# Kernel tuning notes

Hardware: AMD Instinct MI355X
Metric: run time of the kernel (lower is better)

Reference implementation:

```python
import math
import jax, jax.numpy as jnp
import numpy as np

DIM, HEADS, HD = 384, 12, 32
FEAT, WIN, SHIFT = (64, 64), (8, 8), (4, 4)
L = WIN[0] * WIN[1]  # window area = 64
MAX_LOGIT = math.log(1.0 / 0.01)


def _rel_log_coords():
    # pair-wise relative positions, log-spaced (static, numpy)
    coords = np.stack(np.meshgrid(np.arange(WIN[0]), np.arange(WIN[1]), indexing='ij'), 0).reshape(2, -1)
    rel = (coords[:, :, None] - coords[:, None, :]).transpose(1, 2, 0).reshape(-1, 2).astype(np.float32)
    return np.sign(rel) * np.log1p(np.abs(rel))  # [L*L, 2]


def _attn_mask():
    # shifted-window attention mask (static, numpy): 9 regions -> -100 across regions
    H, W = FEAT
    img = np.zeros((H, W), np.int32)
    cnt = 0
    for h0, h1 in ((0, H - WIN[0]), (H - WIN[0], H - SHIFT[0]), (H - SHIFT[0], H)):
        for w0, w1 in ((0, W - WIN[1]), (W - WIN[1], W - SHIFT[1]), (W - SHIFT[1], W)):
            img[h0:h1, w0:w1] = cnt
            cnt += 1
    mw = img.reshape(H // WIN[0], WIN[0], W // WIN[1], WIN[1]).transpose(0, 2, 1, 3).reshape(-1, L)
    diff = mw[:, None, :] - mw[:, :, None]
    return np.where(diff != 0, -100.0, 0.0).astype(np.float32)  # [nW, L, L]


def _ln(x, w, b, eps=1e-5):
    mu = x.mean(-1, keepdims=True)
    var = ((x - mu) ** 2).mean(-1, keepdims=True)
    return (x - mu) / jnp.sqrt(var + eps) * w + b


def setup_inputs() -> dict:
    key = jax.random.key(0)
    ks = jax.random.split(key, 12)
    B = 32
    s = 0.02
    return {
        'x': jax.random.normal(ks[0], (B, FEAT[0], FEAT[1], DIM), jnp.float32),
        'qkv_w': jax.random.normal(ks[1], (3 * DIM, DIM), jnp.float32) * s,
        'qkv_b': jnp.zeros((3 * DIM,), jnp.float32),
        'proj_w': jax.random.normal(ks[2], (DIM, DIM), jnp.float32) * s,
        'proj_b': jnp.zeros((DIM,), jnp.float32),
        'meta_w1': jax.random.normal(ks[3], (384, 2), jnp.float32) * 0.1,
        'meta_b1': jnp.zeros((384,), jnp.float32),
        'meta_w2': jax.random.normal(ks[4], (HEADS, 384), jnp.float32) * 0.1,
        'meta_b2': jnp.zeros((HEADS,), jnp.float32),
        'logit_scale': jnp.full((HEADS,), math.log(10.0), jnp.float32),
        'norm1_w': jnp.ones((DIM,), jnp.float32),
        'norm1_b': jnp.zeros((DIM,), jnp.float32),
        'fc1_w': jax.random.normal(ks[5], (4 * DIM, DIM), jnp.float32) * s,
        'fc1_b': jnp.zeros((4 * DIM,), jnp.float32),
        'fc2_w': jax.random.normal(ks[6], (DIM, 4 * DIM), jnp.float32) * s,
        'fc2_b': jnp.zeros((DIM,), jnp.float32),
        'norm2_w': jnp.ones((DIM,), jnp.float32),
        'norm2_b': jnp.zeros((DIM,), jnp.float32),
    }


def reference(x, qkv_w, qkv_b, proj_w, proj_b, meta_w1, meta_b1, meta_w2, meta_b2,
              logit_scale, norm1_w, norm1_b, fc1_w, fc1_b, fc2_w, fc2_b, norm2_w, norm2_b):
    B, H, W, C = x.shape
    wh, ww = WIN
    # cyclic shift + window partition: (B,H,W,C) -> (B*nW, L, C)
    sx = jnp.roll(x, (-SHIFT[0], -SHIFT[1]), axis=(1, 2))
    xw = sx.reshape(B, H // wh, wh, W // ww, ww, C).transpose(0, 1, 3, 2, 4, 5).reshape(-1, L, C)
    Bw = xw.shape[0]
    qkv = (xw @ qkv_w.T + qkv_b).reshape(Bw, L, 3, HEADS, HD).transpose(2, 0, 3, 1, 4)
    q, k, v = qkv[0], qkv[1], qkv[2]  # [Bw, heads, L, hd]
    # cosine attention
    qn = q / jnp.maximum(jnp.linalg.norm(q, axis=-1, keepdims=True), 1e-12)
    kn = k / jnp.maximum(jnp.linalg.norm(k, axis=-1, keepdims=True), 1e-12)
    attn = jnp.einsum('bhqd,bhkd->bhqk', qn, kn)
    scale = jnp.exp(jnp.minimum(logit_scale, MAX_LOGIT)).reshape(1, HEADS, 1, 1)
    # MLP-based relative position bias
    rel = jnp.asarray(_rel_log_coords())
    bias = jax.nn.relu(rel @ meta_w1.T + meta_b1) @ meta_w2.T + meta_b2  # [L*L, heads]
    bias = bias.T.reshape(HEADS, L, L)
    attn = attn * scale + bias[None]
    # shift mask
    mask = jnp.asarray(_attn_mask())  # [nW, L, L]
    nW = mask.shape[0]
    attn = attn.reshape(Bw // nW, nW, HEADS, L, L) + mask[None, :, None]
    attn = jax.nn.softmax(attn.reshape(Bw, HEADS, L, L), axis=-1)
    out = jnp.einsum('bhqk,bhkd->bhqd', attn, v).transpose(0, 2, 1, 3).reshape(Bw, L, C)
    out = out @ proj_w.T + proj_b
    # window reverse + reverse shift
    out = out.reshape(B, H // wh, W // ww, wh, ww, C).transpose(0, 1, 3, 2, 4, 5).reshape(B, H, W, C)
    out = jnp.roll(out, (SHIFT[0], SHIFT[1]), axis=(1, 2))
    # post-norm residuals (SwinV2Cr style)
    x = x + _ln(out, norm1_w, norm1_b)
    h = jax.nn.gelu(x @ fc1_w.T + fc1_b, approximate=False) @ fc2_w.T + fc2_b
    x = x + _ln(h, norm2_w, norm2_b)
    return x
```

## Files before the change

kernel.cpp:

```cpp
#include <hip/hip_runtime.h>
#include <hip/hip_bf16.h>

typedef __attribute__((ext_vector_type(4))) float f32x4;
typedef __attribute__((ext_vector_type(4))) unsigned int u32x4;
typedef __attribute__((ext_vector_type(8))) __bf16 bf16x8;

#define DEV static __device__ __forceinline__

DEV unsigned short f2bf(float f) {
  unsigned u = __builtin_bit_cast(unsigned, f);
  u += 0x7fffu + ((u >> 16) & 1u);
  return (unsigned short)(u >> 16);
}
DEV float bf2f(unsigned short b) {
  return __builtin_bit_cast(float, ((unsigned)b) << 16);
}
DEV unsigned pk2(float a, float b) {
  return (unsigned)f2bf(a) | ((unsigned)f2bf(b) << 16);
}
DEV unsigned cvtpk(float lo, float hi) {
  unsigned r;
  asm("v_cvt_pk_bf16_f32 %0, %1, %2" : "=v"(r) : "v"(lo), "v"(hi));
  return r;
}
DEV float fexp2(float x) {
  float r;
  asm("v_exp_f32 %0, %1" : "=v"(r) : "v"(x));
  return r;
}
DEV f32x4 mfma16(u32x4 a, u32x4 b, f32x4 c) {
  return __builtin_amdgcn_mfma_f32_16x16x32_bf16(
      __builtin_bit_cast(bf16x8, a), __builtin_bit_cast(bf16x8, b), c, 0, 0, 0);
}
DEV float ssq8(u32x4 c) {
  float s = 0.f;
#pragma unroll
  for (int e = 0; e < 4; e++) {
    float lo = __builtin_bit_cast(float, c[e] << 16);
    float hi = __builtin_bit_cast(float, c[e] & 0xffff0000u);
    s += lo * lo + hi * hi;
  }
  return s;
}
DEV void gload16(const unsigned short* g, unsigned short* l) {
  __builtin_amdgcn_global_load_lds(
      (const __attribute__((address_space(1))) unsigned int*)g,
      (__attribute__((address_space(3))) unsigned int*)l, 16, 0, 0);
}

template <int EPI>
__global__ __launch_bounds__(512, 2) void gemm8(
    const unsigned short* __restrict__ A, const unsigned short* __restrict__ B,
    const float* __restrict__ bias, unsigned short* __restrict__ C,
    int Nc, int K, int nblocks) {
  __shared__ __align__(16) unsigned char smem[131072];
  unsigned short* As0 = (unsigned short*)smem;
  unsigned short* Bs0 = (unsigned short*)(smem + 65536);
  const int bid = blockIdx.x;
  const int mchunk = (gridDim.x >> 3) / nblocks;
  const int xcd = bid & 7, idx = bid >> 3;
  const int nb = idx % nblocks, ml = idx / nblocks;
  const int m0 = (xcd * mchunk + ml) * 256, n0 = nb * 256;
  const int tid = threadIdx.x, w = tid >> 6, l = tid & 63;
  const int lr = l & 15, lg = l >> 4;
  const int wm = (w >> 2) * 128, wn = (w & 3) * 64;
  const int srow = l >> 3;
  const int scol = ((l & 7) ^ srow) * 8;
  const int NT = K >> 6;

  auto stA = [&](int p, int kt, int half, int j) {
    int r = half * 128 + w * 16 + j * 8;
    gload16(A + (size_t)(m0 + r + srow) * K + kt * 64 + scol,
            As0 + p * 16384 + r * 64);
  };
  auto stB = [&](int p, int kt, int half, int j) {
    int r = half * 128 + w * 16 + j * 8;
    gload16(B + (size_t)(n0 + r + srow) * K + kt * 64 + scol,
            Bs0 + p * 16384 + r * 64);
  };

  const f32x4 z4 = {0.f, 0.f, 0.f, 0.f};
  f32x4 acc[8][4];
#pragma unroll
  for (int i = 0; i < 8; i++)
#pragma unroll
    for (int j = 0; j < 4; j++) acc[i][j] = z4;
  u32x4 af[8], bf[8];

#pragma unroll
  for (int ktp = 0; ktp < 2; ktp++) {
    stB(ktp, ktp, 0, 0); stB(ktp, ktp, 0, 1);
    stB(ktp, ktp, 1, 0); stB(ktp, ktp, 1, 1);
    stA(ktp, ktp, 0, 0); stA(ktp, ktp, 0, 1);
    stA(ktp, ktp, 1, 0); stA(ktp, ktp, 1, 1);
  }

  for (int kt = 0; kt < NT; ++kt) {
    const int p = kt & 1;
    if (kt + 1 < NT) {
      asm volatile("s_waitcnt vmcnt(8)" ::: "memory");
    } else {
      asm volatile("s_waitcnt vmcnt(0)" ::: "memory");
    }
    __builtin_amdgcn_s_barrier();

#pragma unroll
    for (int ni = 0; ni < 4; ni++)
#pragma unroll
      for (int ks = 0; ks < 2; ks++) {
        int R = wn + ni * 16 + lr;
        bf[ni * 2 + ks] = *(const u32x4*)&Bs0[p * 16384 + R * 64 +
                                             (((ks * 4 + lg) ^ (lr & 7)) * 8)];
      }
#pragma unroll
    for (int mi = 0; mi < 4; mi++)
#pragma unroll
      for (int ks = 0; ks < 2; ks++) {
        int R = wm + mi * 16 + lr;
        af[mi * 2 + ks] = *(const u32x4*)&As0[p * 16384 + R * 64 +
                                              (((ks * 4 + lg) ^ (lr & 7)) * 8)];
      }
    asm volatile("s_waitcnt lgkmcnt(0)" ::: "memory");
    __builtin_amdgcn_sched_barrier(0);
    __builtin_amdgcn_s_setprio(1);
#pragma unroll
    for (int mi = 0; mi < 4; mi++)
#pragma unroll
      for (int ni = 0; ni < 2; ni++)
#pragma unroll
        for (int ks = 0; ks < 2; ks++)
          acc[mi][ni] = mfma16(bf[ni * 2 + ks], af[mi * 2 + ks], acc[mi][ni]);
    __builtin_amdgcn_s_setprio(0);
    __builtin_amdgcn_s_barrier();

    if (kt + 2 < NT) { stB(p, kt + 2, 0, 0); stB(p, kt + 2, 0, 1); }
    __builtin_amdgcn_s_setprio(1);
#pragma unroll
    for (int mi = 0; mi < 4; mi++)
#pragma unroll
      for (int ni = 0; ni < 2; ni++)
#pragma unroll
        for (int ks = 0; ks < 2; ks++)
          acc[mi][ni + 2] =
              mfma16(bf[(ni + 2) * 2 + ks], af[mi * 2 + ks], acc[mi][ni + 2]);
    __builtin_amdgcn_s_setprio(0);
    __builtin_amdgcn_s_barrier();

#pragma unroll
    for (int mi = 0; mi < 4; mi++)
#pragma unroll
      for (int ks = 0; ks < 2; ks++) {
        int R = wm + 64 + mi * 16 + lr;
        af[mi * 2 + ks] = *(const u32x4*)&As0[p * 16384 + R * 64 +
                                              (((ks * 4 + lg) ^ (lr & 7)) * 8)];
      }
    if (kt + 2 < NT) { stB(p, kt + 2, 1, 0); stB(p, kt + 2, 1, 1); }
    asm volatile("s_waitcnt lgkmcnt(0)" ::: "memory");
    __builtin_amdgcn_sched_barrier(0);
    __builtin_amdgcn_s_setprio(1);
#pragma unroll
    for (int mi = 0; mi < 4; mi++)
#pragma unroll
      for (int ni = 0; ni < 2; ni++)
#pragma unroll
        for (int ks = 0; ks < 2; ks++)
          acc[mi + 4][ni] =
              mfma16(bf[ni * 2 + ks], af[mi * 2 + ks], acc[mi + 4][ni]);
    __builtin_amdgcn_s_setprio(0);
    __builtin_amdgcn_s_barrier();

    if (kt + 2 < NT) {
      stA(p, kt + 2, 0, 0); stA(p, kt + 2, 0, 1);
      stA(p, kt + 2, 1, 0); stA(p, kt + 2, 1, 1);
    }
    __builtin_amdgcn_s_setprio(1);
#pragma unroll
    for (int mi = 0; mi < 4; mi++)
#pragma unroll
      for (int ni = 0; ni < 2; ni++)
#pragma unroll
        for (int ks = 0; ks < 2; ks++)
          acc[mi + 4][ni + 2] =
              mfma16(bf[(ni + 2) * 2 + ks], af[mi * 2 + ks], acc[mi + 4][ni + 2]);
    __builtin_amdgcn_s_setprio(0);
  }

  __builtin_amdgcn_s_barrier();
#pragma unroll
  for (int mh = 0; mh < 2; mh++)
#pragma unroll
    for (int mi = 0; mi < 4; mi++) {
      int mloc = wm + mh * 64 + mi * 16 + lr;
      int msw = mloc & 7;
#pragma unroll
      for (int ni = 0; ni < 4; ni++) {
        f32x4 v = acc[mh * 4 + mi][ni];
        f32x4 bv = *(const f32x4*)&bias[n0 + wn + ni * 16 + lg * 4];
#pragma unroll
        for (int r = 0; r < 4; r++) {
          float t = v[r] + bv[r];
          if (EPI == 1) t = 0.5f * t * (1.0f + erff(t * 0.70710678f));
          v[r] = t;
        }
        int nbyte = (wn + ni * 16 + lg * 4) * 2;
        int addr = mloc * 512 + ((((nbyte >> 4) ^ msw) << 4) | (nbyte & 8));
        *(uint2*)(smem + addr) = make_uint2(cvtpk(v[0], v[1]), cvtpk(v[2], v[3]));
      }
    }
  __syncthreads();
#pragma unroll
  for (int c = 0; c < 16; c++) {
    int m = w * 32 + c * 2 + (l >> 5);
    int h = l & 31;
    u32x4 v = *(const u32x4*)(smem + m * 512 + ((h ^ (m & 7)) << 4));
    int n = n0 + h * 8;
    if (n < Nc) *(u32x4*)&C[(size_t)(m0 + m) * Nc + n] = v;
  }
}

template <int MODE>
__global__ __launch_bounds__(512) void gemm_ln(
    const unsigned short* __restrict__ A, const unsigned short* __restrict__ Bw,
    const float* __restrict__ bias, const float* __restrict__ resf,
    const unsigned short* __restrict__ resb, const float* __restrict__ nw,
    const float* __restrict__ nb, unsigned short* __restrict__ outb,
    float* __restrict__ outf, int K) {
  __shared__ __align__(16) unsigned short As[2][4096];
  __shared__ __align__(16) unsigned short Bs[2][12288];
  const int bid = blockIdx.x;
  const int swz = (bid & 7) * (gridDim.x >> 3) + (bid >> 3);
  const int m0 = swz * 128;
  const int tid = threadIdx.x, w8 = tid >> 6, l = tid & 63;
  const int lr = l & 15, lg = l >> 4;
  const int gsw = (lg ^ ((lr >> 1) & 3)) * 8;
  const int wm2 = (w8 >> 2) * 64;
  const int wn4 = w8 & 3;

  const int rs = l >> 2;
  const int gsrc = ((l & 3) ^ ((l >> 3) & 3)) * 8;
  const unsigned short* g_src[4];
  unsigned short* g_dst[4];
  int g_str[4];
#pragma unroll
  for (int i = 0; i < 4; i++) {
    int g = w8 * 4 + i;
    if (g < 8) {
      g_src[i] = A + (size_t)(m0 + g * 16 + rs) * K + gsrc;
      g_dst[i] = &As[0][g * 512];
      g_str[i] = 4096;
    } else {
      g_src[i] = Bw + (size_t)((g - 8) * 16 + rs) * K + gsrc;
      g_dst[i] = &Bs[0][(g - 8) * 512];
      g_str[i] = 12288;
    }
  }
  auto stage = [&](int buf, int k0) {
#pragma unroll
    for (int i = 0; i < 4; i++) gload16(g_src[i] + k0, g_dst[i] + buf * g_str[i]);
  };

  const f32x4 z4 = {0.f, 0.f, 0.f, 0.f};
  f32x4 acc[4][6];
#pragma unroll
  for (int i = 0; i < 4; i++)
#pragma unroll
    for (int j = 0; j < 6; j++) acc[i][j] = z4;

  auto compute = [&](int buf) {
    u32x4 a[4], b[6];
#pragma unroll
    for (int i = 0; i < 4; i++)
      a[i] = *(const u32x4*)(&As[buf][(wm2 + i * 16 + lr) * 32 + gsw]);
#pragma unroll
    for (int j = 0; j < 6; j++)
      b[j] = *(const u32x4*)(&Bs[buf][(wn4 * 96 + j * 16 + lr) * 32 + gsw]);
#pragma unroll
    for (int i = 0; i < 4; i++)
#pragma unroll
      for (int j = 0; j < 6; j++) acc[i][j] = mfma16(a[i], b[j], acc[i][j]);
  };

  const int nt = K >> 5;
  stage(0, 0);
  for (int t = 0; t < nt; ++t) {
    __syncthreads();
    if (t + 1 < nt) stage((t + 1) & 1, (t + 1) * 32);
    compute(t & 1);
  }

  float bcol[6];
#pragma unroll
  for (int j = 0; j < 6; j++) bcol[j] = bias[wn4 * 96 + j * 16 + lr];
#pragma unroll
  for (int i = 0; i < 4; i++)
#pragma unroll
    for (int j = 0; j < 6; j++)
#pragma unroll
      for (int r = 0; r < 4; r++) acc[i][j][r] += bcol[j];

  float* psum = (float*)(&As[0][0]);
  float* psq  = (float*)(&As[0][1024]);
#pragma unroll
  for (int i = 0; i < 4; i++)
#pragma unroll
    for (int r = 0; r < 4; r++) {
      float s1 = 0.f, s2 = 0.f;
#pragma unroll
      for (int j = 0; j < 6; j++) {
        float v = acc[i][j][r];
        s1 += v;
        s2 += v * v;
      }
#pragma unroll
      for (int d = 1; d < 16; d <<= 1) {
        s1 += __shfl_xor(s1, d, 64);
        s2 += __shfl_xor(s2, d, 64);
      }
      if (lr == 0) {
        int row = wm2 + i * 16 + lg * 4 + r;
        psum[wn4 * 128 + row] = s1;
        psq[wn4 * 128 + row] = s2;
      }
    }
  __syncthreads();

  float wcol[6], b2col[6];
#pragma unroll
  for (int j = 0; j < 6; j++) {
    int col = wn4 * 96 + j * 16 + lr;
    wcol[j] = nw[col];
    b2col[j] = nb[col];
  }
#pragma unroll
  for (int i = 0; i < 4; i++)
#pragma unroll
    for (int r = 0; r < 4; r++) {
      int row = wm2 + i * 16 + lg * 4 + r;
      float sum = psum[row] + psum[128 + row] + psum[256 + row] + psum[384 + row];
      float sq = psq[row] + psq[128 + row] + psq[256 + row] + psq[384 + row];
      float mu = sum * (1.f / 384.f);
      float rstd = rsqrtf(sq * (1.f / 384.f) - mu * mu + 1e-5f);
      size_t nbase;
      if (MODE == 0) {
        int mrow = m0 + row;
        int bb = mrow >> 12, widx = (mrow >> 6) & 63, tt = mrow & 63;
        int yy = (((widx >> 3) << 3) + (tt >> 3) + 4) & 63;
        int xx = (((widx & 7) << 3) + (tt & 7) + 4) & 63;
        nbase = (size_t)((bb << 12) | (yy << 6) | xx) * 384;
      } else {
        nbase = (size_t)(m0 + row) * 384;
      }
#pragma unroll
      for (int j = 0; j < 6; j++) {
        int col = wn4 * 96 + j * 16 + lr;
        float v = (acc[i][j][r] - mu) * rstd * wcol[j] + b2col[j];
        if (MODE == 0) {
          outb[nbase + col] = f2bf(resf[nbase + col] + v);
        } else {
          outf[nbase + col] = bf2f(resb[nbase + col]) + v;
        }
      }
    }
}

__global__ __launch_bounds__(256) void gather_cvt(
    const float* __restrict__ x, unsigned short* __restrict__ xb) {
  int wv = threadIdx.x >> 6, l = threadIdx.x & 63;
  int m = blockIdx.x * 4 + wv;
  int w = m >> 6, t = m & 63;
  int b = w >> 6, wy = (w >> 3) & 7, wx = w & 7;
  int oy = (wy * 8 + (t >> 3) + 4) & 63;
  int ox = (wx * 8 + (t & 7) + 4) & 63;
  const float2* src =
      (const float2*)(x + (size_t)((((b << 6) | oy) << 6) | ox) * 384 + l * 6);
  float2 f0 = src[0], f1 = src[1], f2 = src[2];
  unsigned* dst = (unsigned*)(xb + (size_t)m * 384 + l * 6);
  dst[0] = pk2(f0.x, f0.y);
  dst[1] = pk2(f1.x, f1.y);
  dst[2] = pk2(f2.x, f2.y);
}

__global__ __launch_bounds__(256, 4) void attn_win(
    const unsigned short* __restrict__ qkv, const float* __restrict__ btab2,
    const float* __restrict__ lscale, unsigned short* __restrict__ aout) {
  __shared__ __align__(16) unsigned short vT[4][32 * 72];
  __shared__ __align__(16) float rnk[4][64];
  const int w = blockIdx.x;
  const int wv = threadIdx.x >> 6, l = threadIdx.x & 63;
  const int h = blockIdx.y * 4 + wv;
  const int lr = l & 15, lg = l >> 4;
  const size_t base = (size_t)w * 64 * 1152 + h * 32;
  const f32x4 z4 = {0.f, 0.f, 0.f, 0.f};

  {
    const u32x4* vp = (const u32x4*)(qkv + base + (size_t)l * 1152 + 768);
#pragma unroll
    for (int c4 = 0; c4 < 4; c4++) {
      u32x4 c = vp[c4];
#pragma unroll
      for (int e = 0; e < 4; e++) {
        vT[wv][(c4 * 8 + e * 2) * 72 + l] = (unsigned short)(c[e] & 0xffffu);
        vT[wv][(c4 * 8 + e * 2 + 1) * 72 + l] = (unsigned short)(c[e] >> 16);
      }
    }
  }
  u32x4 kf[4];
#pragma unroll
  for (int tj = 0; tj < 4; tj++) {
    kf[tj] = *(const u32x4*)(qkv + base + (size_t)(tj * 16 + lr) * 1152 + 384 + lg * 8);
    float s = ssq8(kf[tj]);
    s += __shfl_xor(s, 16, 64);
    s += __shfl_xor(s, 32, 64);
    if (lg == 0) rnk[wv][tj * 16 + lr] = rsqrtf(fmaxf(s, 1e-24f));
  }
  u32x4 qf[4];
  float rnq[4];
#pragma unroll
  for (int ti = 0; ti < 4; ti++) {
    qf[ti] = *(const u32x4*)(qkv + base + (size_t)(ti * 16 + lr) * 1152 + lg * 8);
    float s = ssq8(qf[ti]);
    s += __shfl_xor(s, 16, 64);
    s += __shfl_xor(s, 32, 64);
    rnq[ti] = rsqrtf(fmaxf(s, 1e-24f));
  }
  __syncthreads();

  u32x4 vb[2][2];
#pragma unroll
  for (int kc = 0; kc < 2; kc++)
#pragma unroll
    for (int tj2 = 0; tj2 < 2; tj2++)
      vb[kc][tj2] = *(const u32x4*)(&vT[wv][(tj2 * 16 + lr) * 72 + kc * 32 + lg * 8]);

  const float scl2 = expf(fminf(lscale[h], 4.6051702f)) * 1.44269504f;
  const int wt = ((((w >> 3) & 7) == 7) ? 2 : 0) | (((w & 7) == 7) ? 1 : 0);
  const float* tabh = btab2 + (((size_t)wt * 12 + h) << 12);
  const int s0l = lr + ((l & 16) ? 32 : 0);
  const int s1l = s0l + 16;
  const bool hi = (l & 32) != 0;

#pragma unroll
  for (int ti = 0; ti < 4; ti++) {
    f32x4 sv[4];
#pragma unroll
    for (int tj = 0; tj < 4; tj++) sv[tj] = mfma16(kf[tj], qf[ti], z4);
    const float* tab = tabh + ((ti * 16 + lr) << 6);
    const float cb = rnq[ti] * scl2;
    f32x4 val[4];
    float m = -1e30f;
#pragma unroll
    for (int tj = 0; tj < 4; tj++) {
      f32x4 rk4 = *(const f32x4*)(&rnk[wv][tj * 16 + lg * 4]);
      f32x4 t4 = *(const f32x4*)(tab + tj * 16 + lg * 4);
#pragma unroll
      for (int r = 0; r < 4; r++) {
        float v = sv[tj][r] * (cb * rk4[r]) + t4[r];
        val[tj][r] = v;
        m = fmaxf(m, v);
      }
    }
    m = fmaxf(m, __shfl_xor(m, 16, 64));
    m = fmaxf(m, __shfl_xor(m, 32, 64));
    float den = 0.f;
#pragma unroll
    for (int tj = 0; tj < 4; tj++)
#pragma unroll
      for (int r = 0; r < 4; r++) {
        float p = fexp2(val[tj][r] - m);
        val[tj][r] = p;
        den += p;
      }
    den += __shfl_xor(den, 16, 64);
    den += __shfl_xor(den, 32, 64);
    float rden = 1.f / den;
#pragma unroll
    for (int tj = 0; tj < 4; tj++)
#pragma unroll
      for (int r = 0; r < 4; r++) val[tj][r] *= rden;

    f32x4 o[2] = {z4, z4};
#pragma unroll
    for (int kc = 0; kc < 2; kc++) {
      unsigned yA0 = cvtpk(val[2 * kc][0], val[2 * kc][1]);
      unsigned yA1 = cvtpk(val[2 * kc][2], val[2 * kc][3]);
      unsigned yB0 = cvtpk(val[2 * kc + 1][0], val[2 * kc + 1][1]);
      unsigned yB1 = cvtpk(val[2 * kc + 1][2], val[2 * kc + 1][3]);
      unsigned a0 = __shfl((int)yA0, s0l, 64), b0 = __shfl((int)yB0, s0l, 64);
      unsigned a1 = __shfl((int)yA1, s0l, 64), b1 = __shfl((int)yB1, s0l, 64);
      unsigned a2 = __shfl((int)yA0, s1l, 64), b2 = __shfl((int)yB0, s1l, 64);
      unsigned a3 = __shfl((int)yA1, s1l, 64), b3 = __shfl((int)yB1, s1l, 64);
      u32x4 pa = {hi ? b0 : a0, hi ? b1 : a1, hi ? b2 : a2, hi ? b3 : a3};
#pragma unroll
      for (int tj2 = 0; tj2 < 2; tj2++) o[tj2] = mfma16(pa, vb[kc][tj2], o[tj2]);
    }
#pragma unroll
    for (int tj2 = 0; tj2 < 2; tj2++)
#pragma unroll
      for (int r = 0; r < 4; r++)
        aout[(size_t)(w * 64 + ti * 16 + lg * 4 + r) * 384 + h * 32 + tj2 * 16 + lr] =
            f2bf(o[tj2][r]);
  }
}

__global__ __launch_bounds__(256) void btab2_kernel(
    const float* __restrict__ w1, const float* __restrict__ b1,
    const float* __restrict__ w2, const float* __restrict__ b2,
    float* __restrict__ btab2) {
  int p = blockIdx.x * 256 + threadIdx.x;
  int i = p >> 6, j = p & 63;
  float dy = (float)((i >> 3) - (j >> 3));
  float dx = (float)((i & 7) - (j & 7));
  float r0 = (dy > 0.f ? 1.f : (dy < 0.f ? -1.f : 0.f)) * log1pf(fabsf(dy));
  float r1 = (dx > 0.f ? 1.f : (dx < 0.f ? -1.f : 0.f)) * log1pf(fabsf(dx));
  float acc[12];
#pragma unroll
  for (int hh = 0; hh < 12; hh++) acc[hh] = b2[hh];
  for (int c = 0; c < 384; c++) {
    float hv = w1[c * 2] * r0 + w1[c * 2 + 1] * r1 + b1[c];
    hv = fmaxf(hv, 0.f);
#pragma unroll
    for (int hh = 0; hh < 12; hh++) acc[hh] += hv * w2[hh * 384 + c];
  }
  bool ddy = ((i >> 3) >= 4) != ((j >> 3) >= 4);
  bool ddx = ((i & 7) >= 4) != ((j & 7) >= 4);
  const float L2E = 1.44269504f;
#pragma unroll
  for (int wt = 0; wt < 4; wt++) {
    float mask = ((((wt >> 1) != 0) && ddy) || (((wt & 1) != 0) && ddx)) ? -100.f : 0.f;
#pragma unroll
    for (int hh = 0; hh < 12; hh++)
      btab2[(((size_t)wt * 12 + hh) << 12) + p] = (acc[hh] + mask) * L2E;
  }
}

__global__ __launch_bounds__(256) void cvt_kernel(
    const float* __restrict__ s, unsigned short* __restrict__ d, int n) {
  int i = blockIdx.x * 256 + threadIdx.x;
  if (i < n) d[i] = f2bf(s[i]);
}

__global__ __launch_bounds__(256) void cvt_pad_kernel(
    const float* __restrict__ s, unsigned short* __restrict__ d, int n_src,
    int n_tot) {
  int i = blockIdx.x * 256 + threadIdx.x;
  if (i < n_tot) d[i] = (i < n_src) ? f2bf(s[i]) : (unsigned short)0;
}

__global__ __launch_bounds__(256) void pad_bias_kernel(
    const float* __restrict__ s, float* __restrict__ d) {
  int i = blockIdx.x * 256 + threadIdx.x;
  if (i < 1280) d[i] = (i < 1152) ? s[i] : 0.f;
}

extern "C" void kernel_launch(void* const* d_in, const int* in_sizes, int n_in,
                              void* d_out, int out_size, void* d_ws,
                              size_t ws_size, hipStream_t stream) {
  (void)in_sizes; (void)n_in; (void)out_size; (void)ws_size;
  const float* x      = (const float*)d_in[0];
  const float* qkv_w  = (const float*)d_in[1];
  const float* qkv_b  = (const float*)d_in[2];
  const float* proj_w = (const float*)d_in[3];
  const float* proj_b = (const float*)d_in[4];
  const float* mw1    = (const float*)d_in[5];
  const float* mb1    = (const float*)d_in[6];
  const float* mw2    = (const float*)d_in[7];
  const float* mb2    = (const float*)d_in[8];
  const float* lsc    = (const float*)d_in[9];
  const float* n1w    = (const float*)d_in[10];
  const float* n1b    = (const float*)d_in[11];
  const float* w1     = (const float*)d_in[12];
  const float* b1     = (const float*)d_in[13];
  const float* w2     = (const float*)d_in[14];
  const float* b2     = (const float*)d_in[15];
  const float* n2w    = (const float*)d_in[16];
  const float* n2b    = (const float*)d_in[17];

  char* ws = (char*)d_ws;
  unsigned short* wqb  = (unsigned short*)(ws + 0);
  unsigned short* wpb  = (unsigned short*)(ws + 1048576);
  unsigned short* w1b  = (unsigned short*)(ws + 1441792);
  unsigned short* w2b  = (unsigned short*)(ws + 2621440);
  float* qbp           = (float*)(ws + 3801088);
  float* btab2         = (float*)(ws + 3866624);
  unsigned short* xb   = (unsigned short*)(ws + 4718592);
  unsigned short* qkvb = (unsigned short*)(ws + 105381888);
  unsigned short* att  = (unsigned short*)(ws + 440926208);
  unsigned short* hb   = (unsigned short*)(ws + 541589504);
  unsigned short* y1b  = xb;
  float* yout = (float*)d_out;

  cvt_pad_kernel<<<dim3(1920), 256, 0, stream>>>(qkv_w, wqb, 442368, 491520);
  cvt_kernel<<<dim3(576), 256, 0, stream>>>(proj_w, wpb, 147456);
  cvt_kernel<<<dim3(2304), 256, 0, stream>>>(w1, w1b, 589824);
  cvt_kernel<<<dim3(2304), 256, 0, stream>>>(w2, w2b, 589824);
  pad_bias_kernel<<<dim3(5), 256, 0, stream>>>(qkv_b, qbp);
  btab2_kernel<<<dim3(16), 256, 0, stream>>>(mw1, mb1, mw2, mb2, btab2);
  gather_cvt<<<dim3(32768), 256, 0, stream>>>(x, xb);

  gemm8<0><<<dim3(2560), 512, 0, stream>>>(xb, wqb, qbp, qkvb, 1152, 384, 5);
  attn_win<<<dim3(2048, 3), 256, 0, stream>>>(qkvb, btab2, lsc, att);
  gemm_ln<0><<<dim3(1024), 512, 0, stream>>>(
      att, wpb, proj_b, x, nullptr, n1w, n1b, y1b, nullptr, 384);
  for (int c = 0; c < 4; c++) {
    const unsigned short* ya = y1b + (size_t)c * 32768 * 384;
    float* yc = yout + (size_t)c * 32768 * 384;
    gemm8<1><<<dim3(768), 512, 0, stream>>>(ya, w1b, b1, hb, 1536, 384, 6);
    gemm_ln<1><<<dim3(256), 512, 0, stream>>>(
        hb, w2b, b2, nullptr, ya, n2w, n2b, nullptr, yc, 1536);
  }
}
```

Measured before the change: 1.192 ms.

## Rewrite GEMM+LayerNorm with K=64 tiles, deeper prefetch, and unchunked MLP

The fused GEMM+LayerNorm kernel now uses K-tiles of 64 with XOR-swizzled LDS. Global loads for tile kt+2 are issued in pieces between three MFMA phases, with explicit vmcnt waits, barriers and setprio. The MLP stage is no longer split into four batch chunks: one fc1 GEMM covers all rows and writes into the reused qkv buffer, followed by one fc2+LN launch. This is meant to hide memory latency and cut per-iteration sync and launch overhead. In exchange it doubles LDS per block and raises register pressure.

```diff
diff --git a/kernel.cpp b/kernel.cpp
--- a/kernel.cpp
+++ b/kernel.cpp
@@ -219,44 +219,31 @@
 }
 
 template <int MODE>
-__global__ __launch_bounds__(512) void gemm_ln(
+__global__ __launch_bounds__(512, 2) void gemm_ln8(
     const unsigned short* __restrict__ A, const unsigned short* __restrict__ Bw,
     const float* __restrict__ bias, const float* __restrict__ resf,
     const unsigned short* __restrict__ resb, const float* __restrict__ nw,
     const float* __restrict__ nb, unsigned short* __restrict__ outb,
     float* __restrict__ outf, int K) {
-  __shared__ __align__(16) unsigned short As[2][4096];
-  __shared__ __align__(16) unsigned short Bs[2][12288];
+  __shared__ __align__(16) unsigned short As[2][128 * 64];
+  __shared__ __align__(16) unsigned short Bs[2][384 * 64];
   const int bid = blockIdx.x;
   const int swz = (bid & 7) * (gridDim.x >> 3) + (bid >> 3);
   const int m0 = swz * 128;
-  const int tid = threadIdx.x, w8 = tid >> 6, l = tid & 63;
+  const int tid = threadIdx.x, w = tid >> 6, l = tid & 63;
   const int lr = l & 15, lg = l >> 4;
-  const int gsw = (lg ^ ((lr >> 1) & 3)) * 8;
-  const int wm2 = (w8 >> 2) * 64;
-  const int wn4 = w8 & 3;
-
-  const int rs = l >> 2;
-  const int gsrc = ((l & 3) ^ ((l >> 3) & 3)) * 8;
-  const unsigned short* g_src[4];
-  unsigned short* g_dst[4];
-  int g_str[4];
-#pragma unroll
-  for (int i = 0; i < 4; i++) {
-    int g = w8 * 4 + i;
-    if (g < 8) {
-      g_src[i] = A + (size_t)(m0 + g * 16 + rs) * K + gsrc;
-      g_dst[i] = &As[0][g * 512];
-      g_str[i] = 4096;
-    } else {
-      g_src[i] = Bw + (size_t)((g - 8) * 16 + rs) * K + gsrc;
-      g_dst[i] = &Bs[0][(g - 8) * 512];
-      g_str[i] = 12288;
-    }
-  }
-  auto stage = [&](int buf, int k0) {
-#pragma unroll
-    for (int i = 0; i < 4; i++) gload16(g_src[i] + k0, g_dst[i] + buf * g_str[i]);
+  const int wm = (w >> 2) * 64, wn = (w & 3) * 96;
+  const int srow = l >> 3;
+  const int scol = ((l & 7) ^ srow) * 8;
+  const int NT = K >> 6;
+
+  auto stA = [&](int p, int kt, int j) {
+    int r = w * 16 + j * 8;
+    gload16(A + (size_t)(m0 + r + srow) * K + kt * 64 + scol, &As[p][r * 64]);
+  };
+  auto stB = [&](int p, int kt, int part, int j) {
+    int r = part * 192 + w * 24 + j * 8;
+    gload16(Bw + (size_t)(r + srow) * K + kt * 64 + scol, &Bs[p][r * 64]);
   };
 
   const f32x4 z4 = {0.f, 0.f, 0.f, 0.f};
@@ -265,32 +252,86 @@
   for (int i = 0; i < 4; i++)
 #pragma unroll
     for (int j = 0; j < 6; j++) acc[i][j] = z4;
-
-  auto compute = [&](int buf) {
-    u32x4 a[4], b[6];
-#pragma unroll
-    for (int i = 0; i < 4; i++)
-      a[i] = *(const u32x4*)(&As[buf][(wm2 + i * 16 + lr) * 32 + gsw]);
-#pragma unroll
-    for (int j = 0; j < 6; j++)
-      b[j] = *(const u32x4*)(&Bs[buf][(wn4 * 96 + j * 16 + lr) * 32 + gsw]);
-#pragma unroll
-    for (int i = 0; i < 4; i++)
-#pragma unroll
-      for (int j = 0; j < 6; j++) acc[i][j] = mfma16(a[i], b[j], acc[i][j]);
-  };
-
-  const int nt = K >> 5;
-  stage(0, 0);
-  for (int t = 0; t < nt; ++t) {
-    __syncthreads();
-    if (t + 1 < nt) stage((t + 1) & 1, (t + 1) * 32);
-    compute(t & 1);
-  }
-
+  u32x4 af[8], bf[12];
+
+#pragma unroll
+  for (int ktp = 0; ktp < 2; ktp++) {
+    stB(ktp, ktp, 0, 0); stB(ktp, ktp, 0, 1); stB(ktp, ktp, 0, 2);
+    stB(ktp, ktp, 1, 0); stB(ktp, ktp, 1, 1); stB(ktp, ktp, 1, 2);
+    stA(ktp, ktp, 0); stA(ktp, ktp, 1);
+  }
+
+  for (int kt = 0; kt < NT; ++kt) {
+    const int p = kt & 1;
+    if (kt + 1 < NT) {
+      asm volatile("s_waitcnt vmcnt(8)" ::: "memory");
+    } else {
+      asm volatile("s_waitcnt vmcnt(0)" ::: "memory");
+    }
+    __builtin_amdgcn_s_barrier();
+
+#pragma unroll
+    for (int nj = 0; nj < 6; nj++)
+#pragma unroll
+      for (int ks = 0; ks < 2; ks++) {
+        int R = wn + nj * 16 + lr;
+        bf[nj * 2 + ks] =
+            *(const u32x4*)&Bs[p][R * 64 + (((ks * 4 + lg) ^ (lr & 7)) * 8)];
+      }
+#pragma unroll
+    for (int mi = 0; mi < 4; mi++)
+#pragma unroll
+      for (int ks = 0; ks < 2; ks++) {
+        int R = wm + mi * 16 + lr;
+        af[mi * 2 + ks] =
+            *(const u32x4*)&As[p][R * 64 + (((ks * 4 + lg) ^ (lr & 7)) * 8)];
+      }
+    asm volatile("s_waitcnt lgkmcnt(0)" ::: "memory");
+    __builtin_amdgcn_sched_barrier(0);
+    __builtin_amdgcn_s_setprio(1);
+#pragma unroll
+    for (int mi = 0; mi < 4; mi++)
+#pragma unroll
+      for (int nj = 0; nj < 2; nj++)
+#pragma unroll
+        for (int ks = 0; ks < 2; ks++)
+          acc[mi][nj] = mfma16(af[mi * 2 + ks], bf[nj * 2 + ks], acc[mi][nj]);
+    __builtin_amdgcn_s_setprio(0);
+    __builtin_amdgcn_s_barrier();
+
+    if (kt + 2 < NT) {
+      stB(p, kt + 2, 0, 0); stB(p, kt + 2, 0, 1); stB(p, kt + 2, 0, 2);
+    }
+    __builtin_amdgcn_s_setprio(1);
+#pragma unroll
+    for (int mi = 0; mi < 4; mi++)
+#pragma unroll
+      for (int nj = 2; nj < 4; nj++)
+#pragma unroll
+        for (int ks = 0; ks < 2; ks++)
+          acc[mi][nj] = mfma16(af[mi * 2 + ks], bf[nj * 2 + ks], acc[mi][nj]);
+    __builtin_amdgcn_s_setprio(0);
+    __builtin_amdgcn_s_barrier();
+
+    if (kt + 2 < NT) {
+      stB(p, kt + 2, 1, 0); stB(p, kt + 2, 1, 1); stB(p, kt + 2, 1, 2);
+      stA(p, kt + 2, 0); stA(p, kt + 2, 1);
+    }
+    __builtin_amdgcn_s_setprio(1);
+#pragma unroll
+    for (int mi = 0; mi < 4; mi++)
+#pragma unroll
+      for (int nj = 4; nj < 6; nj++)
+#pragma unroll
+        for (int ks = 0; ks < 2; ks++)
+          acc[mi][nj] = mfma16(af[mi * 2 + ks], bf[nj * 2 + ks], acc[mi][nj]);
+    __builtin_amdgcn_s_setprio(0);
+  }
+
+  __syncthreads();
   float bcol[6];
 #pragma unroll
-  for (int j = 0; j < 6; j++) bcol[j] = bias[wn4 * 96 + j * 16 + lr];
+  for (int j = 0; j < 6; j++) bcol[j] = bias[wn + j * 16 + lr];
 #pragma unroll
   for (int i = 0; i < 4; i++)
 #pragma unroll
@@ -300,6 +341,7 @@
 
   float* psum = (float*)(&As[0][0]);
   float* psq  = (float*)(&As[0][1024]);
+  const int wn4 = w & 3;
 #pragma unroll
   for (int i = 0; i < 4; i++)
 #pragma unroll
@@ -317,7 +359,7 @@
         s2 += __shfl_xor(s2, d, 64);
       }
       if (lr == 0) {
-        int row = wm2 + i * 16 + lg * 4 + r;
+        int row = wm + i * 16 + lg * 4 + r;
         psum[wn4 * 128 + row] = s1;
         psq[wn4 * 128 + row] = s2;
       }
@@ -327,7 +369,7 @@
   float wcol[6], b2col[6];
 #pragma unroll
   for (int j = 0; j < 6; j++) {
-    int col = wn4 * 96 + j * 16 + lr;
+    int col = wn + j * 16 + lr;
     wcol[j] = nw[col];
     b2col[j] = nb[col];
   }
@@ -335,7 +377,7 @@
   for (int i = 0; i < 4; i++)
 #pragma unroll
     for (int r = 0; r < 4; r++) {
-      int row = wm2 + i * 16 + lg * 4 + r;
+      int row = wm + i * 16 + lg * 4 + r;
       float sum = psum[row] + psum[128 + row] + psum[256 + row] + psum[384 + row];
       float sq = psq[row] + psq[128 + row] + psq[256 + row] + psq[384 + row];
       float mu = sum * (1.f / 384.f);
@@ -352,7 +394,7 @@
       }
 #pragma unroll
       for (int j = 0; j < 6; j++) {
-        int col = wn4 * 96 + j * 16 + lr;
+        int col = wn + j * 16 + lr;
         float v = (acc[i][j][r] - mu) * rstd * wcol[j] + b2col[j];
         if (MODE == 0) {
           outb[nbase + col] = f2bf(resf[nbase + col] + v);
@@ -585,8 +627,8 @@
   unsigned short* xb   = (unsigned short*)(ws + 4718592);
   unsigned short* qkvb = (unsigned short*)(ws + 105381888);
   unsigned short* att  = (unsigned short*)(ws + 440926208);
-  unsigned short* hb   = (unsigned short*)(ws + 541589504);
   unsigned short* y1b  = xb;
+  unsigned short* hb   = qkvb;
   float* yout = (float*)d_out;
 
   cvt_pad_kernel<<<dim3(1920), 256, 0, stream>>>(qkv_w, wqb, 442368, 491520);
@@ -599,13 +641,9 @@
 
   gemm8<0><<<dim3(2560), 512, 0, stream>>>(xb, wqb, qbp, qkvb, 1152, 384, 5);
   attn_win<<<dim3(2048, 3), 256, 0, stream>>>(qkvb, btab2, lsc, att);
-  gemm_ln<0><<<dim3(1024), 512, 0, stream>>>(
+  gemm_ln8<0><<<dim3(1024), 512, 0, stream>>>(
       att, wpb, proj_b, x, nullptr, n1w, n1b, y1b, nullptr, 384);
-  for (int c = 0; c < 4; c++) {
-    const unsigned short* ya = y1b + (size_t)c * 32768 * 384;
-    float* yc = yout + (size_t)c * 32768 * 384;
-    gemm8<1><<<dim3(768), 512, 0, stream>>>(ya, w1b, b1, hb, 1536, 384, 6);
-    gemm_ln<1><<<dim3(256), 512, 0, stream>>>(
-        hb, w2b, b2, nullptr, ya, n2w, n2b, nullptr, yc, 1536);
-  }
-}
+  gemm8<1><<<dim3(3072), 512, 0, stream>>>(y1b, w1b, b1, hb, 1536, 384, 6);
+  gemm_ln8<1><<<dim3(1024), 512, 0, stream>>>(
+      hb, w2b, b2, nullptr, y1b, n2w, n2b, nullptr, yout, 1536);
+}
```

Result: faster. 1.153 ms (-3.3%).
